# Performance work log

Measured on AMD Instinct MI355X. Metric: run time of the kernel, lower is better.

The kernel has to match this reference:

```python
import jax, jax.numpy as jnp
import numpy as np

B, I, H, O = 65536, 128, 256, 256

def setup_inputs() -> dict:
    key = jax.random.key(0)
    ks = jax.random.split(key, 6)
    s_h = 1.0 / np.sqrt(I + H)
    return {
        "input": jax.random.normal(ks[0], (B, I), jnp.float32),
        "hidden": jax.random.normal(ks[1], (B, H), jnp.float32),
        "w_i2h": jax.random.uniform(ks[2], (4 * H, I + H), jnp.float32, -s_h, s_h),
        "b_i2h": jax.random.uniform(ks[3], (4 * H,), jnp.float32, -s_h, s_h),
        "w_i2o": jax.random.uniform(ks[4], (O, I + H), jnp.float32, -s_h, s_h),
        "b_i2o": jax.random.uniform(ks[5], (O,), jnp.float32, -s_h, s_h),
    }

def reference(input, hidden, w_i2h, b_i2h, w_i2o, b_i2o):
    # combined: [B, I+H]
    combined = jnp.concatenate([input, hidden], axis=1)
    gates = combined @ w_i2h.T + b_i2h            # [B, 4H]
    h, ig, fg, og = jnp.split(gates, 4, axis=1)   # each [B, H]
    ig = jax.nn.sigmoid(ig)
    fg = jax.nn.sigmoid(fg)
    og = jax.nn.sigmoid(og)
    h = jnp.tanh(h)
    new_hidden = og * jnp.tanh(fg * hidden + ig * h)
    output = jax.nn.log_softmax(combined @ w_i2o.T + b_i2o, axis=1)  # [B, O]
    return (output, new_hidden)
```

## Files before the change

### kernel.cpp

```cpp
#include <hip/hip_runtime.h>
#include <hip/hip_bf16.h>
#include <math.h>


typedef __attribute__((ext_vector_type(8))) short bf16x8;
typedef __attribute__((ext_vector_type(4))) float f32x4;

#define BM   64
#define LDA  392
#define NW1  393216
#define NW2  98304

__device__ __forceinline__ unsigned short f2bf(float f) {
    union { __hip_bfloat16 h; unsigned short u; } cv;
    cv.h = __float2bfloat16(f);
    return cv.u;
}
__device__ __forceinline__ float bf2f(unsigned short u) {
    union { __hip_bfloat16 h; unsigned short u; } cv;
    cv.u = u;
    return __bfloat162float(cv.h);
}
__device__ __forceinline__ float fsigmoid(float x) {
    return 1.0f / (1.0f + __expf(-x));
}
__device__ __forceinline__ float ftanh(float x) {
    return 1.0f - 2.0f / (__expf(2.0f * x) + 1.0f);
}

__global__ void conv_w(const float* __restrict__ w1, const float* __restrict__ w2,
                       unsigned short* __restrict__ wb) {
    int idx = blockIdx.x * 256 + threadIdx.x;
    const int n1 = NW1 / 4;
    float4 v;
    if (idx < n1) v = ((const float4*)w1)[idx];
    else          v = ((const float4*)w2)[idx - n1];
    ushort4 u;
    u.x = f2bf(v.x); u.y = f2bf(v.y); u.z = f2bf(v.z); u.w = f2bf(v.w);
    ((ushort4*)wb)[idx] = u;
}

__launch_bounds__(256, 2)
__global__ void lstm_fused(const float* __restrict__ input,
                           const float* __restrict__ hidden,
                           const unsigned short* __restrict__ w1b,
                           const unsigned short* __restrict__ w2b,
                           const float* __restrict__ b1,
                           const float* __restrict__ b2,
                           float* __restrict__ out_ls,
                           float* __restrict__ out_nh)
{
    __shared__ unsigned short A[BM * LDA];
    __shared__ float red_m[4][BM];
    __shared__ float red_s[4][BM];

    const int tid  = threadIdx.x;
    const int wave = tid >> 6;
    const int lane = tid & 63;
    const int l15  = lane & 15;
    const int quad = lane >> 4;
    const size_t r0 = (size_t)blockIdx.x * BM;

    for (int idx = tid; idx < BM * 96; idx += 256) {
        int row = idx / 96, c4 = idx % 96;
        float4 v = (c4 < 32)
            ? ((const float4*)(input  + (r0 + row) * 128))[c4]
            : ((const float4*)(hidden + (r0 + row) * 256))[c4 - 32];
        ushort4 u;
        u.x = f2bf(v.x); u.y = f2bf(v.y); u.z = f2bf(v.z); u.w = f2bf(v.w);
        *(ushort4*)&A[row * LDA + c4 * 4] = u;
    }
    __syncthreads();

    const unsigned short* ap0 = &A[l15 * LDA + quad * 8];

    for (int phase = 0; phase < 5; ++phase) {
        f32x4 acc[4][4];
        #pragma unroll
        for (int i = 0; i < 4; ++i)
            #pragma unroll
            for (int j = 0; j < 4; ++j)
                acc[i][j] = (f32x4){0.f, 0.f, 0.f, 0.f};

        const unsigned short* bp[4];
        if (phase < 4) {
            int j0 = phase * 64 + wave * 16;
            #pragma unroll
            for (int q = 0; q < 4; ++q)
                bp[q] = w1b + (size_t)(q * 256 + j0 + l15) * 384 + quad * 8;
        } else {
            #pragma unroll
            for (int nt = 0; nt < 4; ++nt)
                bp[nt] = w2b + (size_t)(wave * 64 + nt * 16 + l15) * 384 + quad * 8;
        }

        #pragma unroll
        for (int kk = 0; kk < 384; kk += 32) {
            bf16x8 a[4], b[4];
            #pragma unroll
            for (int mt = 0; mt < 4; ++mt)
                a[mt] = *(const bf16x8*)(ap0 + mt * 16 * LDA + kk);
            #pragma unroll
            for (int nt = 0; nt < 4; ++nt)
                b[nt] = *(const bf16x8*)(bp[nt] + kk);
            #pragma unroll
            for (int mt = 0; mt < 4; ++mt)
                #pragma unroll
                for (int nt = 0; nt < 4; ++nt)
                    acc[mt][nt] = __builtin_amdgcn_mfma_f32_16x16x32_bf16(
                        a[mt], b[nt], acc[mt][nt], 0, 0, 0);
        }

        if (phase < 4) {
            int j = phase * 64 + wave * 16 + l15;
            float bq0 = b1[j], bq1 = b1[256 + j], bq2 = b1[512 + j], bq3 = b1[768 + j];
            #pragma unroll
            for (int mt = 0; mt < 4; ++mt) {
                #pragma unroll
                for (int r = 0; r < 4; ++r) {
                    int rowl = mt * 16 + quad * 4 + r;
                    float hprev = bf2f(A[rowl * LDA + 128 + j]);
                    float hv  = ftanh(acc[mt][0][r] + bq0);
                    float igv = fsigmoid(acc[mt][1][r] + bq1);
                    float fgv = fsigmoid(acc[mt][2][r] + bq2);
                    float ogv = fsigmoid(acc[mt][3][r] + bq3);
                    out_nh[(r0 + rowl) * 256 + j] = ogv * ftanh(fgv * hprev + igv * hv);
                }
            }
        } else {
            float bo[4];
            #pragma unroll
            for (int nt = 0; nt < 4; ++nt) bo[nt] = b2[wave * 64 + nt * 16 + l15];
            #pragma unroll
            for (int mt = 0; mt < 4; ++mt)
                #pragma unroll
                for (int nt = 0; nt < 4; ++nt)
                    #pragma unroll
                    for (int r = 0; r < 4; ++r)
                        acc[mt][nt][r] += bo[nt];

            float pm[4][4], ps[4][4];
            #pragma unroll
            for (int mt = 0; mt < 4; ++mt)
                #pragma unroll
                for (int r = 0; r < 4; ++r) {
                    float m = acc[mt][0][r];
                    #pragma unroll
                    for (int nt = 1; nt < 4; ++nt) m = fmaxf(m, acc[mt][nt][r]);
                    pm[mt][r] = m;
                }
            #pragma unroll
            for (int mask = 1; mask < 16; mask <<= 1)
                #pragma unroll
                for (int mt = 0; mt < 4; ++mt)
                    #pragma unroll
                    for (int r = 0; r < 4; ++r)
                        pm[mt][r] = fmaxf(pm[mt][r], __shfl_xor(pm[mt][r], mask, 64));
            #pragma unroll
            for (int mt = 0; mt < 4; ++mt)
                #pragma unroll
                for (int r = 0; r < 4; ++r) {
                    float s = 0.f;
                    #pragma unroll
                    for (int nt = 0; nt < 4; ++nt)
                        s += __expf(acc[mt][nt][r] - pm[mt][r]);
                    ps[mt][r] = s;
                }
            #pragma unroll
            for (int mask = 1; mask < 16; mask <<= 1)
                #pragma unroll
                for (int mt = 0; mt < 4; ++mt)
                    #pragma unroll
                    for (int r = 0; r < 4; ++r)
                        ps[mt][r] += __shfl_xor(ps[mt][r], mask, 64);

            if (l15 == 0) {
                #pragma unroll
                for (int mt = 0; mt < 4; ++mt)
                    #pragma unroll
                    for (int r = 0; r < 4; ++r) {
                        int rowl = mt * 16 + quad * 4 + r;
                        red_m[wave][rowl] = pm[mt][r];
                        red_s[wave][rowl] = ps[mt][r];
                    }
            }
            __syncthreads();
            #pragma unroll
            for (int mt = 0; mt < 4; ++mt)
                #pragma unroll
                for (int r = 0; r < 4; ++r) {
                    int rowl = mt * 16 + quad * 4 + r;
                    float M = red_m[0][rowl];
                    #pragma unroll
                    for (int w = 1; w < 4; ++w) M = fmaxf(M, red_m[w][rowl]);
                    float S = 0.f;
                    #pragma unroll
                    for (int w = 0; w < 4; ++w)
                        S += red_s[w][rowl] * __expf(red_m[w][rowl] - M);
                    float lz = M + logf(S);
                    #pragma unroll
                    for (int nt = 0; nt < 4; ++nt)
                        out_ls[(r0 + rowl) * 256 + wave * 64 + nt * 16 + l15] =
                            acc[mt][nt][r] - lz;
                }
        }
    }
}

extern "C" void kernel_launch(void* const* d_in, const int* in_sizes, int n_in,
                              void* d_out, int out_size, void* d_ws, size_t ws_size,
                              hipStream_t stream) {
    const float* input  = (const float*)d_in[0];
    const float* hidden = (const float*)d_in[1];
    const float* w1     = (const float*)d_in[2];
    const float* b1     = (const float*)d_in[3];
    const float* w2     = (const float*)d_in[4];
    const float* b2     = (const float*)d_in[5];
    float* out = (float*)d_out;
    unsigned short* wb = (unsigned short*)d_ws;

    conv_w<<<dim3((NW1 + NW2) / 4 / 256), dim3(256), 0, stream>>>(w1, w2, wb);
    lstm_fused<<<dim3(65536 / BM), dim3(256), 0, stream>>>(
        input, hidden, wb, wb + NW1, b1, b2,
        out, out + (size_t)65536 * 256);
}
```

Before: 332.0 us.

## Software-pipeline operand loads across phases and use fast rcp/log intrinsics

Double-buffers the A (LDS) and B (global weight) fragments so the next k-step's loads, including the first step of the next phase, are issued before the current MFMAs. Prefetches hidden-state and bias values before the GEMM loop. Also switches sigmoid/tanh division to hardware reciprocal, logf to log2, and restructures the staging loop with packed bf16x2 conversion. This raises register pressure, which may hurt occupancy under the 2-wave launch bounds, and the fast intrinsics slightly reduce accuracy.

```diff
diff --git a/kernel.cpp b/kernel.cpp
--- a/kernel.cpp
+++ b/kernel.cpp
@@ -21,11 +21,14 @@
     cv.u = u;
     return __bfloat162float(cv.h);
 }
+__device__ __forceinline__ float frcp(float x) {
+    return __builtin_amdgcn_rcpf(x);
+}
 __device__ __forceinline__ float fsigmoid(float x) {
-    return 1.0f / (1.0f + __expf(-x));
+    return frcp(1.0f + __expf(-x));
 }
 __device__ __forceinline__ float ftanh(float x) {
-    return 1.0f - 2.0f / (__expf(2.0f * x) + 1.0f);
+    return 1.0f - 2.0f * frcp(__expf(2.0f * x) + 1.0f);
 }
 
 __global__ void conv_w(const float* __restrict__ w1, const float* __restrict__ w2,
@@ -61,65 +64,117 @@
     const int quad = lane >> 4;
     const size_t r0 = (size_t)blockIdx.x * BM;
 
-    for (int idx = tid; idx < BM * 96; idx += 256) {
-        int row = idx / 96, c4 = idx % 96;
-        float4 v = (c4 < 32)
-            ? ((const float4*)(input  + (r0 + row) * 128))[c4]
-            : ((const float4*)(hidden + (r0 + row) * 256))[c4 - 32];
-        ushort4 u;
-        u.x = f2bf(v.x); u.y = f2bf(v.y); u.z = f2bf(v.z); u.w = f2bf(v.w);
-        *(ushort4*)&A[row * LDA + c4 * 4] = u;
+    {
+        const int row = tid >> 2;
+        const int c0  = tid & 3;
+        const float4* si = (const float4*)(input  + (r0 + row) * 128);
+        const float4* sh = (const float4*)(hidden + (r0 + row) * 256);
+        ushort4* dst = (ushort4*)&A[row * LDA];
+        #pragma unroll
+        for (int i = 0; i < 24; ++i) {
+            int c4 = c0 + 4 * i;
+            float4 v = (i < 8) ? si[c4] : sh[c4 - 32];
+            union { __hip_bfloat162 h2; unsigned int u; } p0, p1;
+            p0.h2 = __float22bfloat162_rn(make_float2(v.x, v.y));
+            p1.h2 = __float22bfloat162_rn(make_float2(v.z, v.w));
+            union { ushort4 s4; uint2 u2; } st;
+            st.u2 = make_uint2(p0.u, p1.u);
+            dst[c4] = st.s4;
+        }
     }
     __syncthreads();
 
     const unsigned short* ap0 = &A[l15 * LDA + quad * 8];
 
+    const unsigned short* bp[4];
+    {
+        int j0 = 0 * 64 + wave * 16;
+        #pragma unroll
+        for (int q = 0; q < 4; ++q)
+            bp[q] = w1b + (size_t)(q * 256 + j0 + l15) * 384 + quad * 8;
+    }
+
+    bf16x8 acur[4], bcur[4];
+    #pragma unroll
+    for (int mt = 0; mt < 4; ++mt)
+        acur[mt] = *(const bf16x8*)(ap0 + mt * 16 * LDA);
+    #pragma unroll
+    for (int nt = 0; nt < 4; ++nt)
+        bcur[nt] = *(const bf16x8*)(bp[nt]);
+
+    #pragma unroll 1
     for (int phase = 0; phase < 5; ++phase) {
+        const int j = phase * 64 + wave * 16 + l15;
+        unsigned short hp[16];
+        float bq0, bq1, bq2, bq3;
+        float bo[4];
+        if (phase < 4) {
+            #pragma unroll
+            for (int mt = 0; mt < 4; ++mt)
+                #pragma unroll
+                for (int r = 0; r < 4; ++r)
+                    hp[mt * 4 + r] = A[(mt * 16 + quad * 4 + r) * LDA + 128 + j];
+            bq0 = b1[j]; bq1 = b1[256 + j]; bq2 = b1[512 + j]; bq3 = b1[768 + j];
+        } else {
+            #pragma unroll
+            for (int nt = 0; nt < 4; ++nt) bo[nt] = b2[wave * 64 + nt * 16 + l15];
+        }
+
         f32x4 acc[4][4];
         #pragma unroll
         for (int i = 0; i < 4; ++i)
             #pragma unroll
-            for (int j = 0; j < 4; ++j)
-                acc[i][j] = (f32x4){0.f, 0.f, 0.f, 0.f};
-
-        const unsigned short* bp[4];
+            for (int jj = 0; jj < 4; ++jj)
+                acc[i][jj] = (f32x4){0.f, 0.f, 0.f, 0.f};
+
+        #pragma unroll
+        for (int kk = 0; kk < 12; ++kk) {
+            bf16x8 anxt[4], bnxt[4];
+            if (kk < 11) {
+                #pragma unroll
+                for (int mt = 0; mt < 4; ++mt)
+                    anxt[mt] = *(const bf16x8*)(ap0 + mt * 16 * LDA + (kk + 1) * 32);
+                #pragma unroll
+                for (int nt = 0; nt < 4; ++nt)
+                    bnxt[nt] = *(const bf16x8*)(bp[nt] + (kk + 1) * 32);
+            } else {
+                int pn = phase + 1;
+                if (pn < 4) {
+                    int j0 = pn * 64 + wave * 16;
+                    #pragma unroll
+                    for (int q = 0; q < 4; ++q)
+                        bp[q] = w1b + (size_t)(q * 256 + j0 + l15) * 384 + quad * 8;
+                } else {
+                    #pragma unroll
+                    for (int nt = 0; nt < 4; ++nt)
+                        bp[nt] = w2b + (size_t)(wave * 64 + nt * 16 + l15) * 384 + quad * 8;
+                }
+                #pragma unroll
+                for (int mt = 0; mt < 4; ++mt)
+                    anxt[mt] = *(const bf16x8*)(ap0 + mt * 16 * LDA);
+                #pragma unroll
+                for (int nt = 0; nt < 4; ++nt)
+                    bnxt[nt] = *(const bf16x8*)(bp[nt]);
+            }
+            #pragma unroll
+            for (int mt = 0; mt < 4; ++mt)
+                #pragma unroll
+                for (int nt = 0; nt < 4; ++nt)
+                    acc[mt][nt] = __builtin_amdgcn_mfma_f32_16x16x32_bf16(
+                        acur[mt], bcur[nt], acc[mt][nt], 0, 0, 0);
+            #pragma unroll
+            for (int mt = 0; mt < 4; ++mt) acur[mt] = anxt[mt];
+            #pragma unroll
+            for (int nt = 0; nt < 4; ++nt) bcur[nt] = bnxt[nt];
+        }
+
         if (phase < 4) {
-            int j0 = phase * 64 + wave * 16;
-            #pragma unroll
-            for (int q = 0; q < 4; ++q)
-                bp[q] = w1b + (size_t)(q * 256 + j0 + l15) * 384 + quad * 8;
-        } else {
-            #pragma unroll
-            for (int nt = 0; nt < 4; ++nt)
-                bp[nt] = w2b + (size_t)(wave * 64 + nt * 16 + l15) * 384 + quad * 8;
-        }
-
-        #pragma unroll
-        for (int kk = 0; kk < 384; kk += 32) {
-            bf16x8 a[4], b[4];
-            #pragma unroll
-            for (int mt = 0; mt < 4; ++mt)
-                a[mt] = *(const bf16x8*)(ap0 + mt * 16 * LDA + kk);
-            #pragma unroll
-            for (int nt = 0; nt < 4; ++nt)
-                b[nt] = *(const bf16x8*)(bp[nt] + kk);
-            #pragma unroll
-            for (int mt = 0; mt < 4; ++mt)
-                #pragma unroll
-                for (int nt = 0; nt < 4; ++nt)
-                    acc[mt][nt] = __builtin_amdgcn_mfma_f32_16x16x32_bf16(
-                        a[mt], b[nt], acc[mt][nt], 0, 0, 0);
-        }
-
-        if (phase < 4) {
-            int j = phase * 64 + wave * 16 + l15;
-            float bq0 = b1[j], bq1 = b1[256 + j], bq2 = b1[512 + j], bq3 = b1[768 + j];
             #pragma unroll
             for (int mt = 0; mt < 4; ++mt) {
                 #pragma unroll
                 for (int r = 0; r < 4; ++r) {
                     int rowl = mt * 16 + quad * 4 + r;
-                    float hprev = bf2f(A[rowl * LDA + 128 + j]);
+                    float hprev = bf2f(hp[mt * 4 + r]);
                     float hv  = ftanh(acc[mt][0][r] + bq0);
                     float igv = fsigmoid(acc[mt][1][r] + bq1);
                     float fgv = fsigmoid(acc[mt][2][r] + bq2);
@@ -128,9 +183,6 @@
                 }
             }
         } else {
-            float bo[4];
-            #pragma unroll
-            for (int nt = 0; nt < 4; ++nt) bo[nt] = b2[wave * 64 + nt * 16 + l15];
             #pragma unroll
             for (int mt = 0; mt < 4; ++mt)
                 #pragma unroll
@@ -197,7 +249,7 @@
                     #pragma unroll
                     for (int w = 0; w < 4; ++w)
                         S += red_s[w][rowl] * __expf(red_m[w][rowl] - M);
-                    float lz = M + logf(S);
+                    float lz = M + 0.69314718055994531f * __log2f(S);
                     #pragma unroll
                     for (int nt = 0; nt < 4; ++nt)
                         out_ls[(r0 + rowl) * 256 + wave * 64 + nt * 16 + l15] =
```

Measured after the change: 333.8 us. Within noise of the previous version (+0.6%).
